# Performance work log

Hardware: AMD Instinct MI355X
Metric: run time of the kernel (lower is better)

Reference implementation:

```python
import jax, jax.numpy as jnp
import numpy as np

NUM_HEADS = 8
EMBED_DIM = 512
EXPAND = 3
RPE_DIM = 512
RPE_LAYERS = 3
B, N = 4, 2048
D1 = (EXPAND * EMBED_DIM) // NUM_HEADS * NUM_HEADS  # 1536
HEAD_DIM = D1 // NUM_HEADS  # 192


def srms(x):
    # SimpleRMSNorm: x / (||x||_2 * d^{-1/2} + eps)
    d = x.shape[-1]
    rms = jnp.linalg.norm(x, axis=-1, keepdims=True) * (d ** -0.5)
    return x / (rms + 1e-8)


def rpe_net(idx, Wp, bp, Wl, bl, Wr, br):
    # idx: (m, 1) relative positions -> (m, h*head_dim)
    h = idx @ Wp.T + bp
    for i in range(Wl.shape[0]):  # fixed small layer count
        h = jax.nn.relu(srms(h)) @ Wl[i].T + bl[i]
    return jax.nn.relu(srms(h)) @ Wr.T + br


def setup_inputs() -> dict:
    key = jax.random.key(0)
    ks = jax.random.split(key, 12)
    s = 0.02
    return {
        "x": jax.random.normal(ks[0], (B, N, EMBED_DIM), jnp.float32),
        "Wu": jax.random.normal(ks[1], (D1, EMBED_DIM), jnp.float32) * s,
        "bu": jnp.zeros((D1,), jnp.float32),
        "Wv": jax.random.normal(ks[2], (D1, EMBED_DIM), jnp.float32) * s,
        "bv": jnp.zeros((D1,), jnp.float32),
        "Wo": jax.random.normal(ks[3], (EMBED_DIM, D1), jnp.float32) * s,
        "bo": jnp.zeros((EMBED_DIM,), jnp.float32),
        "Wp": jax.random.normal(ks[4], (RPE_DIM, 1), jnp.float32) * s,
        "bp": jax.random.normal(ks[5], (RPE_DIM,), jnp.float32) * s,
        "Wl": jax.random.normal(ks[6], (RPE_LAYERS, RPE_DIM, RPE_DIM), jnp.float32) * s,
        "bl": jax.random.normal(ks[7], (RPE_LAYERS, RPE_DIM), jnp.float32) * s,
        "Wr": jax.random.normal(ks[8], (NUM_HEADS * HEAD_DIM, RPE_DIM), jnp.float32) * s,
        "br": jax.random.normal(ks[9], (NUM_HEADS * HEAD_DIM,), jnp.float32) * s,
    }


def reference(x, Wu, bu, Wv, bv, Wo, bo, Wp, bp, Wl, bl, Wr, br):
    b, n, e = x.shape
    d1 = Wu.shape[0]
    hd = d1 // NUM_HEADS
    u = jax.nn.silu(x @ Wu.T + bu)                       # (b, n, d1)
    v = jax.nn.silu(x @ Wv.T + bv)                       # (b, n, d1)
    v = v.reshape(b, n, NUM_HEADS, hd).transpose(0, 2, 1, 3)  # (b, h, n, d)
    # Tno non-causal, par_type=1: indices [0, 1..n-1, 0, -(n-1)..-1]
    pos = jnp.arange(1, n, dtype=x.dtype)
    zero = jnp.zeros((1,), x.dtype)
    idx = jnp.concatenate([zero, pos, zero, -pos[::-1]])[:, None]  # (2n, 1)
    a = rpe_net(idx, Wp, bp, Wl, bl, Wr, br)             # (2n, h*d)
    a = a.reshape(2 * n, NUM_HEADS, hd).transpose(1, 0, 2)  # (h, 2n, d)
    m = 2 * n
    # circular conv of length 2n along sequence, truncate to n
    y = jnp.fft.rfft(v, m, axis=2) * jnp.fft.rfft(a, m, axis=1)[None]
    out = jnp.fft.irfft(y, m, axis=2)[:, :, :n, :]       # (b, h, n, d)
    out = out.transpose(0, 2, 1, 3).reshape(b, n, d1)    # (b, n, d1)
    return (u * out) @ Wo.T + bo
```

## Files before the change

### kernel.cpp

```cpp
#include <hip/hip_runtime.h>

#define N_SEQ 2048
#define M_FFT 4096
#define D1    1536
#define NH    8
#define HD    192
#define ED    512

typedef __bf16 bf16;
typedef __bf16 bf16x2 __attribute__((ext_vector_type(2)));
typedef __bf16 bf16x4 __attribute__((ext_vector_type(4)));
typedef __bf16 bf16x8 __attribute__((ext_vector_type(8)));
typedef float  floatx4 __attribute__((ext_vector_type(4)));

enum { MODE_PLAIN = 0, MODE_SILU_UV = 1, MODE_AT = 3 };

__device__ __forceinline__ void gload16(const void* g, void* l) {
    __builtin_amdgcn_global_load_lds(
        (const __attribute__((address_space(1))) void*)g,
        (__attribute__((address_space(3))) void*)l, 16, 0, 0);
}

template<int MODE, typename OutT>
__global__ __launch_bounds__(256) void gemm_bf16(
    const bf16* __restrict__ A, const bf16* __restrict__ Bw,
    const float* __restrict__ bias, const float* __restrict__ bias2,
    OutT* __restrict__ C, OutT* __restrict__ C2,
    int M, int Nc, int K)
{
    __shared__ __align__(16) bf16 As[128 * 32];
    __shared__ __align__(16) bf16 Bs[128 * 32];

    const int tid  = threadIdx.x;
    const int row0 = blockIdx.y * 128;
    const int col0 = blockIdx.x * 128;
    const int wid  = tid >> 6;
    const int lane = tid & 63;
    const int lm   = lane & 15;
    const int lk   = lane >> 4;
    const int wm   = wid >> 1;
    const int wn   = wid & 1;
    const int ldrow  = tid >> 2;
    const int ldcol8 = (tid & 3) * 8;

    floatx4 acc[4][4] = {};

    const bf16* Ag = A  + ((size_t)(row0 + ldrow)) * K + ldcol8;
    const bf16* Bg = Bw + ((size_t)(col0 + ldrow)) * K + ldcol8;
    bf16* AsW = As + (wid * 16) * 32;
    bf16* BsW = Bs + (wid * 16) * 32;

    for (int k0 = 0; k0 < K; k0 += 32) {
        gload16(Ag + k0, AsW);
        gload16(Ag + (size_t)64 * K + k0, AsW + 64 * 32);
        gload16(Bg + k0, BsW);
        gload16(Bg + (size_t)64 * K + k0, BsW + 64 * 32);
        __syncthreads();

        bf16x8 af[4], bfr[4];
        #pragma unroll
        for (int mi = 0; mi < 4; ++mi)
            af[mi] = *(const bf16x8*)&As[(wm * 64 + mi * 16 + lm) * 32 + lk * 8];
        #pragma unroll
        for (int nj = 0; nj < 4; ++nj)
            bfr[nj] = *(const bf16x8*)&Bs[(wn * 64 + nj * 16 + lm) * 32 + lk * 8];
        #pragma unroll
        for (int mi = 0; mi < 4; ++mi)
            #pragma unroll
            for (int nj = 0; nj < 4; ++nj)
                acc[mi][nj] = __builtin_amdgcn_mfma_f32_16x16x32_bf16(
                    af[mi], bfr[nj], acc[mi][nj], 0, 0, 0);
        __syncthreads();
    }

    const float* bs = bias;
    OutT* dst = C;
    int cadj = 0;
    if (MODE == MODE_SILU_UV && col0 >= D1) { bs = bias2; dst = C2; cadj = D1; }

    float bcol[4];
    #pragma unroll
    for (int nj = 0; nj < 4; ++nj)
        bcol[nj] = bs[col0 - cadj + wn * 64 + nj * 16 + lm];

    #pragma unroll
    for (int mi = 0; mi < 4; ++mi) {
        const int rbase = row0 + wm * 64 + mi * 16 + lk * 4;
        #pragma unroll
        for (int nj = 0; nj < 4; ++nj) {
            const int col = col0 - cadj + wn * 64 + nj * 16 + lm;
            float vals[4];
            #pragma unroll
            for (int r = 0; r < 4; ++r) {
                float val = acc[mi][nj][r] + bcol[nj];
                if (MODE == MODE_SILU_UV)
                    val = val / (1.0f + __expf(-val));
                vals[r] = val;
            }
            if (MODE == MODE_SILU_UV) {
                int b = rbase >> 11, s = rbase & 2047;
                bf16x4 o;
                #pragma unroll
                for (int r = 0; r < 4; ++r) o[r] = (bf16)vals[r];
                *(bf16x4*)&((bf16*)dst)[((size_t)(b * D1 + col)) * N_SEQ + s] = o;
            } else if (MODE == MODE_AT) {
                float4 o = make_float4(vals[0], vals[1], vals[2], vals[3]);
                *(float4*)&((float*)C)[(size_t)col * M + rbase] = o;
            } else {
                #pragma unroll
                for (int r = 0; r < 4; ++r)
                    C[(size_t)(rbase + r) * Nc + col] = (OutT)vals[r];
            }
        }
    }
}

__global__ __launch_bounds__(256) void f2b_all_kernel(
    const float* __restrict__ x,  const float* __restrict__ s0,
    const float* __restrict__ s1, const float* __restrict__ s2,
    const float* __restrict__ s3, const float* __restrict__ s4,
    bf16* __restrict__ x_bf, bf16* __restrict__ w_bf)
{
    const int bid = blockIdx.x;
    const float* src;
    bf16* dst;
    size_t off;
    if (bid < 4096) {
        src = x; dst = x_bf; off = (size_t)bid * 1024;
    } else {
        int t = bid - 4096;
        int seg = t / 768;
        src = seg == 0 ? s0 : seg == 1 ? s1 : seg == 2 ? s2 : seg == 3 ? s3 : s4;
        dst = w_bf + (size_t)seg * 786432;
        off = (size_t)(t % 768) * 1024;
    }
    size_t i = off + (size_t)threadIdx.x * 4;
    float4 f = *(const float4*)(src + i);
    union { bf16 h[4]; short4 s; } u4;
    u4.h[0] = (bf16)f.x; u4.h[1] = (bf16)f.y;
    u4.h[2] = (bf16)f.z; u4.h[3] = (bf16)f.w;
    *(short4*)(dst + i) = u4.s;
}

__global__ __launch_bounds__(256) void rpe_in_srms_kernel(
    const float* __restrict__ Wp, const float* __restrict__ bp,
    bf16* __restrict__ g)
{
    const int j = blockIdx.x;
    const int tid = threadIdx.x;
    float idxv = (j < N_SEQ) ? (float)j
                             : (j == N_SEQ ? 0.0f : (float)(j - 2 * N_SEQ));
    float h1 = idxv * Wp[tid] + bp[tid];
    float h2 = idxv * Wp[tid + 256] + bp[tid + 256];
    float ss = h1 * h1 + h2 * h2;
    #pragma unroll
    for (int off = 32; off > 0; off >>= 1) ss += __shfl_down(ss, off, 64);
    __shared__ float red[4];
    if ((tid & 63) == 0) red[tid >> 6] = ss;
    __syncthreads();
    float tot = red[0] + red[1] + red[2] + red[3];
    float scale = 1.0f / (sqrtf(tot) * 0.04419417382415922f + 1e-8f);
    g[(size_t)j * ED + tid]       = (bf16)fmaxf(h1 * scale, 0.0f);
    g[(size_t)j * ED + tid + 256] = (bf16)fmaxf(h2 * scale, 0.0f);
}

__global__ __launch_bounds__(256) void srms_relu_kernel(
    const float* __restrict__ in, bf16* __restrict__ out)
{
    const int row = blockIdx.x;
    const int tid = threadIdx.x;
    const float* p = in + (size_t)row * ED;

    float ss = 0.0f;
    for (int i = tid; i < ED; i += 256) { float x = p[i]; ss += x * x; }
    #pragma unroll
    for (int off = 32; off > 0; off >>= 1) ss += __shfl_down(ss, off, 64);
    __shared__ float red[4];
    if ((tid & 63) == 0) red[tid >> 6] = ss;
    __syncthreads();
    float tot = red[0] + red[1] + red[2] + red[3];
    float scale = 1.0f / (sqrtf(tot) * 0.04419417382415922f + 1e-8f);
    for (int i = tid; i < ED; i += 256)
        out[(size_t)row * ED + i] = (bf16)fmaxf(p[i] * scale, 0.0f);
}

#define FFT_LDS_SZ 4381
#define CC1 0.9238795325112867f
#define SS1 0.3826834323650898f
#define RR2 0.7071067811865476f

__device__ __forceinline__ int fpad(int i) { return i + (i >> 4) + 2 * (i >> 8); }

__device__ __forceinline__ float2 cmul(float2 a, float2 b) {
    return make_float2(a.x * b.x - a.y * b.y, a.x * b.y + a.y * b.x);
}
__device__ __forceinline__ float2 cadd(float2 a, float2 b) {
    return make_float2(a.x + b.x, a.y + b.y);
}
__device__ __forceinline__ float2 csub(float2 a, float2 b) {
    return make_float2(a.x - b.x, a.y - b.y);
}
__device__ __forceinline__ float2 cneg_i(float2 a) { return make_float2(a.y, -a.x); }
__device__ __forceinline__ float2 cpos_i(float2 a) { return make_float2(-a.y, a.x); }
__host__ __device__ constexpr int brev4(int t) {
    return ((t & 1) << 3) | ((t & 2) << 1) | ((t & 4) >> 1) | ((t & 8) >> 3);
}

template<bool HZ>
__device__ __forceinline__ void fft16_dif_r4(float2 x[16]) {
    const float2 W1 = make_float2( CC1, -SS1);
    const float2 W2 = make_float2( RR2, -RR2);
    const float2 W3 = make_float2( SS1, -CC1);
    const float2 W6 = make_float2(-RR2, -RR2);
    const float2 W9 = make_float2(-CC1,  SS1);
    #pragma unroll
    for (int n = 0; n < 4; ++n) {
        float2 A, B, C, D;
        if (HZ) { A = x[n]; C = x[n]; B = x[n + 4]; D = x[n + 4]; }
        else {
            A = cadd(x[n], x[n + 8]);  C = csub(x[n], x[n + 8]);
            B = cadd(x[n + 4], x[n + 12]); D = csub(x[n + 4], x[n + 12]);
        }
        float2 s = csub(A, B);
        float2 nid = cneg_i(D);
        float2 m = cadd(C, nid);
        float2 p = csub(C, nid);
        x[n] = cadd(A, B);
        if (n == 0)      { x[4] = s;            x[8]  = m;           x[12] = p; }
        else if (n == 1) { x[5] = cmul(s, W2);  x[9]  = cmul(m, W1); x[13] = cmul(p, W3); }
        else if (n == 2) { x[6] = cneg_i(s);    x[10] = cmul(m, W2); x[14] = cmul(p, W6); }
        else             { x[7] = cmul(s, W6);  x[11] = cmul(m, W3); x[15] = cmul(p, W9); }
    }
    #pragma unroll
    for (int q = 0; q < 16; q += 4) {
        float2 a = x[q], b = x[q + 1], c = x[q + 2], d = x[q + 3];
        float2 a1 = cadd(a, c), c1 = csub(a, c);
        float2 b1 = cadd(b, d), d1 = cneg_i(csub(b, d));
        x[q]     = cadd(a1, b1);
        x[q + 1] = csub(a1, b1);
        x[q + 2] = cadd(c1, d1);
        x[q + 3] = csub(c1, d1);
    }
}

template<bool HALF_OUT>
__device__ __forceinline__ void fft16_dit_inv_r4(float2 x[16]) {
    const float2 V1 = make_float2( CC1, SS1);
    const float2 V2 = make_float2( RR2, RR2);
    const float2 V3 = make_float2( SS1, CC1);
    const float2 V6 = make_float2(-RR2, RR2);
    #pragma unroll
    for (int q = 0; q < 16; q += 4) {
        float2 a = x[q], b = x[q + 1], c = x[q + 2], d = x[q + 3];
        float2 a1 = cadd(a, b), b1 = csub(a, b);
        float2 c1 = cadd(c, d), d1 = csub(c, d);
        float2 t = cpos_i(d1);
        x[q]     = cadd(a1, c1);
        x[q + 2] = csub(a1, c1);
        x[q + 1] = cadd(b1, t);
        x[q + 3] = csub(b1, t);
    }
    #pragma unroll
    for (int n = 0; n < 4; ++n) {
        float2 t1, t2;
        if (n == 0)      { t1 = x[4];             t2 = x[12]; }
        else if (n == 1) { t1 = cmul(x[5],  V2);  t2 = cmul(x[13], V2); }
        else if (n == 2) { t1 = cpos_i(x[6]);     t2 = cpos_i(x[14]); }
        else             { t1 = cmul(x[7],  V6);  t2 = cmul(x[15], V6); }
        float2 P = cadd(x[n], t1), Q = csub(x[n], t1);
        float2 R = cadd(x[n + 8], t2), S = csub(x[n + 8], t2);
        float2 t, u;
        if (n == 0)      { t = R;            u = S; }
        else if (n == 1) { t = cmul(R, V1);  u = cmul(S, V1); }
        else if (n == 2) { t = cmul(R, V2);  u = cmul(S, V2); }
        else             { t = cmul(R, V3);  u = cmul(S, V3); }
        float2 iu = cpos_i(u);
        x[n]     = cadd(P, t);
        x[n + 4] = cadd(Q, iu);
        if (!HALF_OUT) {
            x[n + 8]  = csub(P, t);
            x[n + 12] = csub(Q, iu);
        }
    }
}

__device__ __forceinline__ void stage_twiddle_tree(
    float2 v[16], int j, float rden, float sgn)
{
    float s, c;
    __sincosf(sgn * 6.283185307179586f * (float)j * rden, &s, &c);
    float2 w[16];
    w[1] = make_float2(c, s);
    w[2] = cmul(w[1], w[1]);
    w[3] = cmul(w[1], w[2]);
    w[4] = cmul(w[2], w[2]);
    w[5] = cmul(w[1], w[4]);
    w[6] = cmul(w[2], w[4]);
    w[7] = cmul(w[3], w[4]);
    w[8] = cmul(w[4], w[4]);
    #pragma unroll
    for (int t = 9; t < 16; ++t) w[t] = cmul(w[t - 8], w[8]);
    #pragma unroll
    for (int tau = 1; tau < 16; ++tau)
        v[brev4(tau)] = cmul(v[brev4(tau)], w[tau]);
}

template<bool HALF_ZERO>
__device__ void fft4096_fwd(float2* d, int tid)
{
    float2 v[16];
    {
        const int j = tid;
        if (HALF_ZERO) {
            #pragma unroll
            for (int t = 0; t < 8; ++t) v[t] = d[fpad(j + (t << 8))];
            fft16_dif_r4<true>(v);
        } else {
            #pragma unroll
            for (int t = 0; t < 16; ++t) v[t] = d[fpad(j + (t << 8))];
            fft16_dif_r4<false>(v);
        }
        stage_twiddle_tree(v, j, 1.0f / 4096.0f, -1.0f);
        #pragma unroll
        for (int p = 0; p < 16; ++p) d[fpad(j + (p << 8))] = v[p];
    }
    __syncthreads();
    {
        const int base = ((tid >> 4) << 8) + (tid & 15);
        #pragma unroll
        for (int t = 0; t < 16; ++t) v[t] = d[fpad(base + (t << 4))];
        fft16_dif_r4<false>(v);
        stage_twiddle_tree(v, tid & 15, 1.0f / 256.0f, -1.0f);
        #pragma unroll
        for (int p = 0; p < 16; ++p) d[fpad(base + (p << 4))] = v[p];
    }
    __syncthreads();
    {
        const int base = tid << 4;
        #pragma unroll
        for (int t = 0; t < 16; ++t) v[t] = d[fpad(base + t)];
        fft16_dif_r4<false>(v);
        #pragma unroll
        for (int p = 0; p < 16; ++p) d[fpad(base + p)] = v[p];
    }
    __syncthreads();
}

__global__ __launch_bounds__(256) void fft_a_kernel(
    const float* __restrict__ a_t, float2* __restrict__ Wspec)
{
    __shared__ float2 data[FFT_LDS_SZ];
    const int tid = threadIdx.x;
    const int h = blockIdx.x / 96, dp = blockIdx.x % 96;

    const float* r0 = a_t + ((size_t)(h * HD + 2 * dp)) * M_FFT;
    const float* r1 = r0 + M_FFT;

    for (int j = tid; j < 4096; j += 256) data[fpad(j)] = make_float2(r0[j], r1[j]);
    __syncthreads();
    fft4096_fwd<false>(data, tid);

    float2* outrow = Wspec + (size_t)blockIdx.x * 4096;
    for (int j = tid; j < 4096; j += 256) outrow[j] = data[fpad(j)];
}

__global__ __launch_bounds__(256) void fft_conv_kernel(
    const bf16* __restrict__ v_t, const float2* __restrict__ Wspec,
    const bf16* __restrict__ u_t, bf16* __restrict__ gated_t)
{
    __shared__ float2 data[FFT_LDS_SZ];
    const int tid = threadIdx.x;
    const int bx = blockIdx.x;
    const int b  = bx / 768;
    const int r  = bx % 768;
    const int h  = r / 96, dp = r % 96;
    const int ch = h * HD + 2 * dp;

    const bf16* z0 = v_t + ((size_t)(b * D1 + ch)) * N_SEQ;
    const bf16* z1 = z0 + N_SEQ;

    {
        const int s = tid * 8;
        bf16x8 a0 = *(const bf16x8*)(z0 + s);
        bf16x8 a1 = *(const bf16x8*)(z1 + s);
        #pragma unroll
        for (int i = 0; i < 8; ++i)
            data[fpad(s + i)] = make_float2((float)a0[i], (float)a1[i]);
    }
    __syncthreads();

    fft4096_fwd<true>(data, tid);

    const float2* Wrow = Wspec + (size_t)r * 4096;
    float2 v[16];
    {
        const int base = tid << 4;
        #pragma unroll
        for (int i = 0; i < 16; ++i) {
            const int p  = base + i;
            const int k  = __brev((unsigned)p) >> 20;
            const int km = (4096 - k) & 4095;
            const int p2 = __brev((unsigned)km) >> 20;
            float2 Zk = data[fpad(p)];
            float2 Zm = data[fpad(p2)];
            float2 Wk = Wrow[p];
            float2 Wm = Wrow[p2];
            float2 V0 = make_float2(0.5f * (Zk.x + Zm.x), 0.5f * (Zk.y - Zm.y));
            float2 V1 = make_float2(0.5f * (Zk.y + Zm.y), 0.5f * (Zm.x - Zk.x));
            float2 A0 = make_float2(0.5f * (Wk.x + Wm.x), 0.5f * (Wk.y - Wm.y));
            float2 A1 = make_float2(0.5f * (Wk.y + Wm.y), 0.5f * (Wm.x - Wk.x));
            float2 P = cmul(V0, A0), Q = cmul(V1, A1);
            v[i] = make_float2(P.x - Q.y, P.y + Q.x);
        }
        __syncthreads();
        fft16_dit_inv_r4<false>(v);
        #pragma unroll
        for (int i = 0; i < 16; ++i) data[fpad(base + i)] = v[i];
    }
    __syncthreads();
    {
        const int base = ((tid >> 4) << 8) + (tid & 15);
        #pragma unroll
        for (int p = 0; p < 16; ++p) v[p] = data[fpad(base + (p << 4))];
        stage_twiddle_tree(v, tid & 15, 1.0f / 256.0f, 1.0f);
        fft16_dit_inv_r4<false>(v);
        #pragma unroll
        for (int t = 0; t < 16; ++t) data[fpad(base + (t << 4))] = v[t];
    }
    __syncthreads();
    {
        const int j = tid;
        #pragma unroll
        for (int p = 0; p < 16; ++p) v[p] = data[fpad(j + (p << 8))];
        stage_twiddle_tree(v, j, 1.0f / 4096.0f, 1.0f);
        fft16_dit_inv_r4<true>(v);
        #pragma unroll
        for (int t = 0; t < 8; ++t) data[fpad(j + (t << 8))] = v[t];
    }
    __syncthreads();

    const float inv_m = 1.0f / 4096.0f;
    const bf16* u0 = u_t + ((size_t)(b * D1 + ch)) * N_SEQ;
    const bf16* u1 = u0 + N_SEQ;
    bf16* g0 = gated_t + ((size_t)(b * D1 + ch)) * N_SEQ;
    bf16* g1 = g0 + N_SEQ;
    {
        const int t = tid * 8;
        bf16x8 ua = *(const bf16x8*)(u0 + t);
        bf16x8 ub = *(const bf16x8*)(u1 + t);
        bf16x8 oa, ob;
        #pragma unroll
        for (int i = 0; i < 8; ++i) {
            float2 y = data[fpad(t + i)];
            oa[i] = (bf16)(y.x * inv_m * (float)ua[i]);
            ob[i] = (bf16)(y.y * inv_m * (float)ub[i]);
        }
        *(bf16x8*)(g0 + t) = oa;
        *(bf16x8*)(g1 + t) = ob;
    }
}

__global__ __launch_bounds__(256) void transpose_cs_kernel(
    const bf16* __restrict__ in, bf16* __restrict__ outp)
{
    __shared__ bf16 tile[64 * 68];
    const int c0 = blockIdx.x * 64;
    const int m0 = blockIdx.y * 64;
    const int b  = m0 >> 11;
    const int s0 = m0 & 2047;
    const int tid = threadIdx.x;
    const int cl = tid >> 4;
    const int sc = (tid & 15) * 4;
    #pragma unroll
    for (int p = 0; p < 4; ++p) {
        int c = p * 16 + cl;
        bf16x4 v = *(const bf16x4*)&in[((size_t)(b * D1 + c0 + c)) * N_SEQ + s0 + sc];
        *(bf16x4*)&tile[c * 68 + sc] = v;
    }
    __syncthreads();
    const int sl = tid >> 4;
    const int cc = (tid & 15) * 4;
    #pragma unroll
    for (int p = 0; p < 4; ++p) {
        int s = p * 16 + sl;
        bf16x4 o;
        #pragma unroll
        for (int j = 0; j < 4; ++j) o[j] = tile[(cc + j) * 68 + s];
        *(bf16x4*)&outp[((size_t)(m0 + s)) * D1 + c0 + cc] = o;
    }
}

extern "C" void kernel_launch(void* const* d_in, const int* in_sizes, int n_in,
                              void* d_out, int out_size, void* d_ws, size_t ws_size,
                              hipStream_t stream)
{
    const float* x  = (const float*)d_in[0];
    const float* Wu = (const float*)d_in[1];
    const float* bu = (const float*)d_in[2];
    const float* Wv = (const float*)d_in[3];
    const float* bv = (const float*)d_in[4];
    const float* Wo = (const float*)d_in[5];
    const float* bo = (const float*)d_in[6];
    const float* Wp = (const float*)d_in[7];
    const float* bp = (const float*)d_in[8];
    const float* Wl = (const float*)d_in[9];
    const float* bl = (const float*)d_in[10];
    const float* Wr = (const float*)d_in[11];
    const float* br = (const float*)d_in[12];
    float* out = (float*)d_out;

    float* ws      = (float*)d_ws;
    float* a_t     = ws;
    float* Wspec   = a_t   + 6291456;
    float* h0      = Wspec + 6291456;
    bf16*  bfws    = (bf16*)(h0 + 2097152);
    bf16*  x_bf    = bfws;
    bf16*  w_bf    = x_bf    + 4194304;
    bf16*  Wuv_bf  = w_bf;
    bf16*  Wo_bf   = w_bf    + 2 * 786432;
    bf16*  Wl_bf   = Wo_bf   + 786432;
    bf16*  Wr_bf   = Wl_bf   + 786432;
    bf16*  g_bf    = Wr_bf   + 786432;
    bf16*  u_t     = g_bf    + 2097152;
    bf16*  v_t     = u_t     + 12582912;
    bf16*  gated_t = v_t     + 12582912;
    bf16*  gated   = gated_t + 12582912;

    dim3 blk(256);

    f2b_all_kernel<<<4096 + 5 * 768, blk, 0, stream>>>(
        x, Wu, Wv, Wo, Wl, Wr, x_bf, w_bf);

    gemm_bf16<MODE_SILU_UV, bf16><<<dim3(24, 64), blk, 0, stream>>>(
        x_bf, Wuv_bf, bu, bv, u_t, v_t, 8192, 2 * D1, ED);

    rpe_in_srms_kernel<<<4096, blk, 0, stream>>>(Wp, bp, g_bf);
    for (int i = 0; i < 3; ++i) {
        gemm_bf16<MODE_PLAIN, float><<<dim3(4, 32), blk, 0, stream>>>(
            g_bf, Wl_bf + (size_t)i * ED * ED, bl + (size_t)i * ED, nullptr,
            h0, nullptr, 4096, ED, ED);
        srms_relu_kernel<<<4096, blk, 0, stream>>>(h0, g_bf);
    }
    gemm_bf16<MODE_AT, float><<<dim3(12, 32), blk, 0, stream>>>(
        g_bf, Wr_bf, br, nullptr, a_t, nullptr, 4096, D1, ED);

    fft_a_kernel<<<768, blk, 0, stream>>>(a_t, (float2*)Wspec);
    fft_conv_kernel<<<3072, blk, 0, stream>>>(
        v_t, (const float2*)Wspec, u_t, gated_t);

    transpose_cs_kernel<<<dim3(24, 128), blk, 0, stream>>>(gated_t, gated);

    gemm_bf16<MODE_PLAIN, float><<<dim3(4, 64), blk, 0, stream>>>(
        gated, Wo_bf, bo, nullptr, out, nullptr, 8192, ED, D1);
}
```

Baseline: 365.5 us.

## Fuse RPE MLP chain into a single kernel with per-row SRMS folding

```diff
diff --git a/kernel.cpp b/kernel.cpp
--- a/kernel.cpp
+++ b/kernel.cpp
@@ -8,12 +8,11 @@
 #define ED    512
 
 typedef __bf16 bf16;
-typedef __bf16 bf16x2 __attribute__((ext_vector_type(2)));
 typedef __bf16 bf16x4 __attribute__((ext_vector_type(4)));
 typedef __bf16 bf16x8 __attribute__((ext_vector_type(8)));
 typedef float  floatx4 __attribute__((ext_vector_type(4)));
 
-enum { MODE_PLAIN = 0, MODE_SILU_UV = 1, MODE_AT = 3 };
+enum { MODE_PLAIN = 0, MODE_SILU_UV = 1 };
 
 __device__ __forceinline__ void gload16(const void* g, void* l) {
     __builtin_amdgcn_global_load_lds(
@@ -103,9 +102,6 @@
                 #pragma unroll
                 for (int r = 0; r < 4; ++r) o[r] = (bf16)vals[r];
                 *(bf16x4*)&((bf16*)dst)[((size_t)(b * D1 + col)) * N_SEQ + s] = o;
-            } else if (MODE == MODE_AT) {
-                float4 o = make_float4(vals[0], vals[1], vals[2], vals[3]);
-                *(float4*)&((float*)C)[(size_t)col * M + rbase] = o;
             } else {
                 #pragma unroll
                 for (int r = 0; r < 4; ++r)
@@ -122,6 +118,7 @@
     bf16* __restrict__ x_bf, bf16* __restrict__ w_bf)
 {
     const int bid = blockIdx.x;
+    const int tid = threadIdx.x;
     const float* src;
     bf16* dst;
     size_t off;
@@ -130,11 +127,12 @@
     } else {
         int t = bid - 4096;
         int seg = t / 768;
-        src = seg == 0 ? s0 : seg == 1 ? s1 : seg == 2 ? s2 : seg == 3 ? s3 : s4;
+        src = seg == 0 ? s0 : seg == 1 ? s1 : seg == 2 ? s2
+            : seg == 3 ? s3 : s4;
         dst = w_bf + (size_t)seg * 786432;
         off = (size_t)(t % 768) * 1024;
     }
-    size_t i = off + (size_t)threadIdx.x * 4;
+    size_t i = off + (size_t)tid * 4;
     float4 f = *(const float4*)(src + i);
     union { bf16 h[4]; short4 s; } u4;
     u4.h[0] = (bf16)f.x; u4.h[1] = (bf16)f.y;
@@ -142,46 +140,132 @@
     *(short4*)(dst + i) = u4.s;
 }
 
-__global__ __launch_bounds__(256) void rpe_in_srms_kernel(
+__global__ __launch_bounds__(256) void rpe_mega_kernel(
     const float* __restrict__ Wp, const float* __restrict__ bp,
-    bf16* __restrict__ g)
-{
-    const int j = blockIdx.x;
-    const int tid = threadIdx.x;
-    float idxv = (j < N_SEQ) ? (float)j
-                             : (j == N_SEQ ? 0.0f : (float)(j - 2 * N_SEQ));
-    float h1 = idxv * Wp[tid] + bp[tid];
-    float h2 = idxv * Wp[tid + 256] + bp[tid + 256];
-    float ss = h1 * h1 + h2 * h2;
-    #pragma unroll
-    for (int off = 32; off > 0; off >>= 1) ss += __shfl_down(ss, off, 64);
-    __shared__ float red[4];
-    if ((tid & 63) == 0) red[tid >> 6] = ss;
-    __syncthreads();
-    float tot = red[0] + red[1] + red[2] + red[3];
-    float scale = 1.0f / (sqrtf(tot) * 0.04419417382415922f + 1e-8f);
-    g[(size_t)j * ED + tid]       = (bf16)fmaxf(h1 * scale, 0.0f);
-    g[(size_t)j * ED + tid + 256] = (bf16)fmaxf(h2 * scale, 0.0f);
-}
-
-__global__ __launch_bounds__(256) void srms_relu_kernel(
-    const float* __restrict__ in, bf16* __restrict__ out)
-{
-    const int row = blockIdx.x;
-    const int tid = threadIdx.x;
-    const float* p = in + (size_t)row * ED;
-
-    float ss = 0.0f;
-    for (int i = tid; i < ED; i += 256) { float x = p[i]; ss += x * x; }
-    #pragma unroll
-    for (int off = 32; off > 0; off >>= 1) ss += __shfl_down(ss, off, 64);
-    __shared__ float red[4];
-    if ((tid & 63) == 0) red[tid >> 6] = ss;
-    __syncthreads();
-    float tot = red[0] + red[1] + red[2] + red[3];
-    float scale = 1.0f / (sqrtf(tot) * 0.04419417382415922f + 1e-8f);
-    for (int i = tid; i < ED; i += 256)
-        out[(size_t)row * ED + i] = (bf16)fmaxf(p[i] * scale, 0.0f);
+    const bf16* __restrict__ Wl_bf, const float* __restrict__ bl,
+    const bf16* __restrict__ Wr_bf, const float* __restrict__ br,
+    float* __restrict__ a_t)
+{
+    __shared__ __align__(16) bf16 hA[32][520];
+    __shared__ float red[4][32];
+    __shared__ float sums[32];
+
+    const int tid  = threadIdx.x;
+    const int w    = tid >> 6;
+    const int lane = tid & 63;
+    const int lm   = lane & 15;
+    const int lk   = lane >> 4;
+    const int r0   = blockIdx.x * 32;
+
+    {
+        const int c1 = tid, c2 = tid + 256;
+        const float wp1 = Wp[c1], wp2 = Wp[c2];
+        const float b1 = bp[c1], b2 = bp[c2];
+        for (int j = 0; j < 32; ++j) {
+            int jg = r0 + j;
+            float idxv = (jg < N_SEQ) ? (float)jg
+                       : (jg == N_SEQ ? 0.0f : (float)(jg - 2 * N_SEQ));
+            float v1 = idxv * wp1 + b1;
+            float v2 = idxv * wp2 + b2;
+            float ss = v1 * v1 + v2 * v2;
+            #pragma unroll
+            for (int m = 1; m < 64; m <<= 1) ss += __shfl_xor(ss, m, 64);
+            if (lane == 0) red[w][j] = ss;
+            hA[j][c1] = (bf16)fmaxf(v1, 0.0f);
+            hA[j][c2] = (bf16)fmaxf(v2, 0.0f);
+        }
+    }
+    __syncthreads();
+    if (tid < 32) sums[tid] = red[0][tid] + red[1][tid] + red[2][tid] + red[3][tid];
+    __syncthreads();
+
+    for (int l = 0; l < 3; ++l) {
+        const bf16* W = Wl_bf + (size_t)l * ED * ED;
+        const float* bias = bl + (size_t)l * ED;
+        const int colw = w * 128;
+
+        floatx4 acc[2][8] = {};
+        for (int k0 = 0; k0 < ED; k0 += 32) {
+            bf16x8 af0 = *(const bf16x8*)&hA[lm][k0 + lk * 8];
+            bf16x8 af1 = *(const bf16x8*)&hA[16 + lm][k0 + lk * 8];
+            #pragma unroll
+            for (int nj = 0; nj < 8; ++nj) {
+                const int col = colw + nj * 16 + lm;
+                bf16x8 bfr = *(const bf16x8*)&W[(size_t)col * ED + k0 + lk * 8];
+                acc[0][nj] = __builtin_amdgcn_mfma_f32_16x16x32_bf16(
+                    af0, bfr, acc[0][nj], 0, 0, 0);
+                acc[1][nj] = __builtin_amdgcn_mfma_f32_16x16x32_bf16(
+                    af1, bfr, acc[1][nj], 0, 0, 0);
+            }
+        }
+        float bcol[8];
+        #pragma unroll
+        for (int nj = 0; nj < 8; ++nj) bcol[nj] = bias[colw + nj * 16 + lm];
+
+        __syncthreads();
+        #pragma unroll
+        for (int mi = 0; mi < 2; ++mi) {
+            #pragma unroll
+            for (int r = 0; r < 4; ++r) {
+                const int row = mi * 16 + lk * 4 + r;
+                float sc = 1.0f / (sqrtf(sums[row]) * 0.04419417382415922f + 1e-8f);
+                float ss = 0.0f;
+                float vv[8];
+                #pragma unroll
+                for (int nj = 0; nj < 8; ++nj) {
+                    float val = acc[mi][nj][r] * sc + bcol[nj];
+                    ss += val * val;
+                    vv[nj] = fmaxf(val, 0.0f);
+                }
+                #pragma unroll
+                for (int nj = 0; nj < 8; ++nj)
+                    hA[row][colw + nj * 16 + lm] = (bf16)vv[nj];
+                ss += __shfl_xor(ss, 1, 64);
+                ss += __shfl_xor(ss, 2, 64);
+                ss += __shfl_xor(ss, 4, 64);
+                ss += __shfl_xor(ss, 8, 64);
+                if (lm == 0) red[w][row] = ss;
+            }
+        }
+        __syncthreads();
+        if (tid < 32) sums[tid] = red[0][tid] + red[1][tid] + red[2][tid] + red[3][tid];
+        __syncthreads();
+    }
+
+    for (int ch = 0; ch < 3; ++ch) {
+        const int colw = w * 384 + ch * 128;
+        floatx4 acc[2][8] = {};
+        for (int k0 = 0; k0 < ED; k0 += 32) {
+            bf16x8 af0 = *(const bf16x8*)&hA[lm][k0 + lk * 8];
+            bf16x8 af1 = *(const bf16x8*)&hA[16 + lm][k0 + lk * 8];
+            #pragma unroll
+            for (int nj = 0; nj < 8; ++nj) {
+                const int col = colw + nj * 16 + lm;
+                bf16x8 bfr = *(const bf16x8*)&Wr_bf[(size_t)col * ED + k0 + lk * 8];
+                acc[0][nj] = __builtin_amdgcn_mfma_f32_16x16x32_bf16(
+                    af0, bfr, acc[0][nj], 0, 0, 0);
+                acc[1][nj] = __builtin_amdgcn_mfma_f32_16x16x32_bf16(
+                    af1, bfr, acc[1][nj], 0, 0, 0);
+            }
+        }
+        #pragma unroll
+        for (int mi = 0; mi < 2; ++mi) {
+            #pragma unroll
+            for (int nj = 0; nj < 8; ++nj) {
+                const int col = colw + nj * 16 + lm;
+                const float bb = br[col];
+                float4 o;
+                float* op = &o.x;
+                #pragma unroll
+                for (int r = 0; r < 4; ++r) {
+                    const int row = mi * 16 + lk * 4 + r;
+                    float sc = 1.0f / (sqrtf(sums[row]) * 0.04419417382415922f + 1e-8f);
+                    op[r] = acc[mi][nj][r] * sc + bb;
+                }
+                *(float4*)&a_t[(size_t)col * M_FFT + r0 + mi * 16 + lk * 4] = o;
+            }
+        }
+    }
 }
 
 #define FFT_LDS_SZ 4381
@@ -512,16 +596,14 @@
     float* ws      = (float*)d_ws;
     float* a_t     = ws;
     float* Wspec   = a_t   + 6291456;
-    float* h0      = Wspec + 6291456;
-    bf16*  bfws    = (bf16*)(h0 + 2097152);
+    bf16*  bfws    = (bf16*)(Wspec + 6291456);
     bf16*  x_bf    = bfws;
     bf16*  w_bf    = x_bf    + 4194304;
     bf16*  Wuv_bf  = w_bf;
     bf16*  Wo_bf   = w_bf    + 2 * 786432;
     bf16*  Wl_bf   = Wo_bf   + 786432;
     bf16*  Wr_bf   = Wl_bf   + 786432;
-    bf16*  g_bf    = Wr_bf   + 786432;
-    bf16*  u_t     = g_bf    + 2097152;
+    bf16*  u_t     = Wr_bf   + 786432;
     bf16*  v_t     = u_t     + 12582912;
     bf16*  gated_t = v_t     + 12582912;
     bf16*  gated   = gated_t + 12582912;
@@ -534,15 +616,8 @@
     gemm_bf16<MODE_SILU_UV, bf16><<<dim3(24, 64), blk, 0, stream>>>(
         x_bf, Wuv_bf, bu, bv, u_t, v_t, 8192, 2 * D1, ED);
 
-    rpe_in_srms_kernel<<<4096, blk, 0, stream>>>(Wp, bp, g_bf);
-    for (int i = 0; i < 3; ++i) {
-        gemm_bf16<MODE_PLAIN, float><<<dim3(4, 32), blk, 0, stream>>>(
-            g_bf, Wl_bf + (size_t)i * ED * ED, bl + (size_t)i * ED, nullptr,
-            h0, nullptr, 4096, ED, ED);
-        srms_relu_kernel<<<4096, blk, 0, stream>>>(h0, g_bf);
-    }
-    gemm_bf16<MODE_AT, float><<<dim3(12, 32), blk, 0, stream>>>(
-        g_bf, Wr_bf, br, nullptr, a_t, nullptr, 4096, D1, ED);
+    rpe_mega_kernel<<<128, blk, 0, stream>>>(
+        Wp, bp, Wl_bf, bl, Wr_bf, br, a_t);
 
     fft_a_kernel<<<768, blk, 0, stream>>>(a_t, (float2*)Wspec);
     fft_conv_kernel<<<3072, blk, 0, stream>>>(
```

Result: slower. 438.3 us (+19.9%).
